# Performance work log

Hardware: AMD Instinct MI355X
Metric: run time of the kernel (lower is better)

## Reference

```python
import math
import jax, jax.numpy as jnp
import numpy as np

K = 4          # beats_per_bar
POS_DIM = 32   # fourier pos-embed dim


def setup_inputs() -> dict:
    key = jax.random.key(0)
    k1, k2, k3 = jax.random.split(key, 3)
    B, M, D = 8, 8192, 1024
    beat_emb = jax.random.normal(k1, (B, M, D), dtype=jnp.float32)
    W = jax.random.normal(k2, (D, D + POS_DIM), dtype=jnp.float32) * 0.02  # nn.Linear weight [out, in]
    b = jax.random.normal(k3, (D,), dtype=jnp.float32) * 0.02
    return {"beat_emb": beat_emb, "W": W, "b": b}


def _fourier_features(pos, dim):
    # pos: [Mb] in [0,1] -> [Mb, dim] (dim even, so no zero-pad branch needed)
    half = dim // 2
    freqs = jnp.exp(jnp.linspace(0.0, math.log(1000.0), half)).astype(pos.dtype)
    ang = pos[:, None] * freqs  # [Mb, half]
    return jnp.concatenate([jnp.sin(ang), jnp.cos(ang)], axis=-1)


def reference(beat_emb, W, b):
    B, M, D = beat_emb.shape
    Mb = (M + K - 1) // K
    pad = Mb * K - M
    x = jnp.pad(beat_emb, ((0, 0), (0, pad), (0, 0))) if pad else beat_emb
    # fused segment mean: [B, Mb, K, D] -> sum -> divide by actual segment length
    sums = x.reshape(B, Mb, K, D).sum(axis=2)
    counts = jnp.minimum(K, M - jnp.arange(Mb) * K).astype(beat_emb.dtype)  # [Mb]
    out = sums / counts[None, :, None]  # [B, Mb, D]
    # fourier positional features on normalized bar index (same for every batch row)
    idx = jnp.arange(Mb, dtype=beat_emb.dtype)
    pos = jnp.clip(idx / max(1, Mb - 1), 0.0, 1.0)
    ff = _fourier_features(pos, POS_DIM)                     # [Mb, POS_DIM]
    ff = jnp.broadcast_to(ff[None], (B, Mb, POS_DIM))
    h = jnp.concatenate([out, ff], axis=-1)                  # [B, Mb, D+POS_DIM]
    return jnp.einsum('bmi,oi->bmo', h, W) + b               # Linear: x @ W.T + b
```

## Files before the change

### kernel.cpp

```cpp
#include <hip/hip_runtime.h>
#include <math.h>
#include <stdint.h>
#include <stddef.h>

typedef short bf16x8 __attribute__((ext_vector_type(8)));
typedef short bf16x4 __attribute__((ext_vector_type(4)));
typedef float f32x4  __attribute__((ext_vector_type(4)));

#define BATCH   8
#define D       1024
#define POSD    32
#define WIN     1056
#define MBARS   2048
#define MROWS   16384
#define NOUT    1024

__device__ __forceinline__ short f2bf(float f) {
    unsigned u = __builtin_bit_cast(unsigned, f);
    u += 0x7fffu + ((u >> 16) & 1u);
    return (short)(u >> 16);
}

__device__ __forceinline__ void async_load16(const short* g, short* l) {
    __builtin_amdgcn_global_load_lds((__attribute__((address_space(1))) void*)g,
                                     (__attribute__((address_space(3))) void*)l,
                                     16, 0, 0);
}

__global__ __launch_bounds__(256) void prep2(const float* __restrict__ W,
                                             const float* __restrict__ bias,
                                             short* __restrict__ Wb,
                                             float* __restrict__ FFW) {
    const int t   = threadIdx.x;
    const int bid = blockIdx.x;
    if (bid < NOUT) {
        const float* wr = W + (size_t)bid * WIN;
        float4 v = ((const float4*)wr)[t];
        bf16x4 o = { f2bf(v.x), f2bf(v.y), f2bf(v.z), f2bf(v.w) };
        *(bf16x4*)(Wb + (size_t)bid * D + t * 4) = o;
    } else {
        const int mb0 = (bid - NOUT) * 8;
        __shared__ float ff[8][32];
        if (t < 32) {
            float fr = expf((float)(t & 15) * (6.907755278982137f / 15.0f));
#pragma unroll
            for (int e = 0; e < 8; ++e) {
                float pos = (float)(mb0 + e) * (1.0f / (float)(MBARS - 1));
                float ang = pos * fr;
                ff[e][t] = (t < 16) ? sinf(ang) : cosf(ang);
            }
        }
        __syncthreads();
#pragma unroll
        for (int u = 0; u < 4; ++u) {
            const int n = t + u * 256;
            const float* wp = W + (size_t)n * WIN + D;
            float4 wv[8];
#pragma unroll
            for (int blk = 0; blk < 8; ++blk) wv[blk] = ((const float4*)wp)[blk];
            const float bn = bias[n];
#pragma unroll
            for (int e = 0; e < 8; ++e) {
                float s = bn;
#pragma unroll
                for (int blk = 0; blk < 8; ++blk) {
                    s += ff[e][blk * 4 + 0] * wv[blk].x + ff[e][blk * 4 + 1] * wv[blk].y
                       + ff[e][blk * 4 + 2] * wv[blk].z + ff[e][blk * 4 + 3] * wv[blk].w;
                }
                FFW[(size_t)(mb0 + e) * NOUT + n] = s;
            }
        }
    }
}

__global__ __launch_bounds__(512, 2) void fused(const float* __restrict__ x,
                                                const short* __restrict__ Wb,
                                                const float* __restrict__ FFW,
                                                float* __restrict__ out) {
    __shared__ short As[64 * 64];
    __shared__ short Bs[1024 * 64];

    const int tid  = threadIdx.x;
    const int wave = tid >> 6;
    const int lane = tid & 63;
    const int m0   = blockIdx.x * 64;

    const int ra = tid >> 3;
    const int oa = tid & 7;
    const float* xg = x + (size_t)(m0 + ra) * 4096 + oa * 8;
    short* aw = As + ra * 64 + ((oa ^ (ra & 7)) << 3);
    const short* bg = Wb + (size_t)ra * D + ((oa ^ (ra & 7)) << 3);
    short* bl = Bs + wave * 512;

    const int r  = lane & 15;
    const int q  = lane >> 4;
    const int rx = r & 7;
    const short* afr = As + r * 64;
    const short* bfr = Bs + (wave * 128 + r) * 64;
    const int sl0 = ((q    ) ^ rx) << 3;
    const int sl1 = ((4 + q) ^ rx) << 3;

    f32x4 acc[4][8] = {};

    for (int k0 = 0; k0 < D; k0 += 64) {
        __syncthreads();
        float4 t00 = *(const float4*)(xg + k0);
        float4 t01 = *(const float4*)(xg + k0 + 4);
        float4 t10 = *(const float4*)(xg + k0 + 1024);
        float4 t11 = *(const float4*)(xg + k0 + 1028);
        float4 t20 = *(const float4*)(xg + k0 + 2048);
        float4 t21 = *(const float4*)(xg + k0 + 2052);
        float4 t30 = *(const float4*)(xg + k0 + 3072);
        float4 t31 = *(const float4*)(xg + k0 + 3076);
#pragma unroll
        for (int i = 0; i < 16; ++i)
            async_load16(bg + k0 + (size_t)i * 64 * D, bl + i * 4096);
        bf16x8 av = { f2bf((t00.x + t10.x + t20.x + t30.x) * 0.25f),
                      f2bf((t00.y + t10.y + t20.y + t30.y) * 0.25f),
                      f2bf((t00.z + t10.z + t20.z + t30.z) * 0.25f),
                      f2bf((t00.w + t10.w + t20.w + t30.w) * 0.25f),
                      f2bf((t01.x + t11.x + t21.x + t31.x) * 0.25f),
                      f2bf((t01.y + t11.y + t21.y + t31.y) * 0.25f),
                      f2bf((t01.z + t11.z + t21.z + t31.z) * 0.25f),
                      f2bf((t01.w + t11.w + t21.w + t31.w) * 0.25f) };
        *(bf16x8*)aw = av;
        __syncthreads();

#pragma unroll
        for (int s = 0; s < 2; ++s) {
            const int sl = s ? sl1 : sl0;
            bf16x8 a[4], b[8];
#pragma unroll
            for (int i = 0; i < 4; ++i) a[i] = *(const bf16x8*)(afr + i * 1024 + sl);
#pragma unroll
            for (int j = 0; j < 8; ++j) b[j] = *(const bf16x8*)(bfr + j * 1024 + sl);
#pragma unroll
            for (int i = 0; i < 4; ++i)
#pragma unroll
                for (int j = 0; j < 8; ++j)
                    acc[i][j] = __builtin_amdgcn_mfma_f32_16x16x32_bf16(a[i], b[j], acc[i][j], 0, 0, 0);
        }
    }

    const int mbb = m0 & (MBARS - 1);
    const int c0  = wave * 128 + r;
    const int rt0 = q << 2;
#pragma unroll
    for (int i = 0; i < 4; ++i)
#pragma unroll
        for (int rg = 0; rg < 4; ++rg) {
            const int rt = i * 16 + rt0 + rg;
            const float* fw = FFW + (size_t)(mbb + rt) * NOUT + c0;
            float* cp = out + (size_t)(m0 + rt) * NOUT + c0;
#pragma unroll
            for (int j = 0; j < 8; ++j)
                cp[j * 16] = acc[i][j][rg] + fw[j * 16];
        }
}

extern "C" void kernel_launch(void* const* d_in, const int* in_sizes, int n_in,
                              void* d_out, int out_size, void* d_ws, size_t ws_size,
                              hipStream_t stream) {
    const float* x    = (const float*)d_in[0];
    const float* W    = (const float*)d_in[1];
    const float* bias = (const float*)d_in[2];
    float* out = (float*)d_out;

    short* Wb  = (short*)d_ws;
    float* FFW = (float*)((char*)d_ws + (size_t)NOUT * D * sizeof(short));

    prep2<<<dim3(NOUT + MBARS / 8), dim3(256), 0, stream>>>(W, bias, Wb, FFW);
    fused<<<dim3(MROWS / 64), dim3(512), 0, stream>>>(x, Wb, FFW, out);
}
```

Measured before the change: 466.3 us.

## Double-buffer A tile and read W fragments directly from global memory

Drops the large LDS staging buffer for the bf16 weight matrix. Each wave now loads its B fragments straight from global memory (through L2 and cache). The pooled activation tile is double-buffered in LDS, so the next K-slice of x is fetched while the MFMAs run on the current one, and the loop needs only one barrier per iteration. This cuts LDS use a lot, which may allow higher occupancy. The cost is that every wave reissues uncoalesced-ish global loads for W on each iteration, with latency exposed to the MFMA loop.

```diff
diff --git a/kernel.cpp b/kernel.cpp
--- a/kernel.cpp
+++ b/kernel.cpp
@@ -19,12 +19,6 @@
     unsigned u = __builtin_bit_cast(unsigned, f);
     u += 0x7fffu + ((u >> 16) & 1u);
     return (short)(u >> 16);
-}
-
-__device__ __forceinline__ void async_load16(const short* g, short* l) {
-    __builtin_amdgcn_global_load_lds((__attribute__((address_space(1))) void*)g,
-                                     (__attribute__((address_space(3))) void*)l,
-                                     16, 0, 0);
 }
 
 __global__ __launch_bounds__(256) void prep2(const float* __restrict__ W,
@@ -77,8 +71,7 @@
                                                 const short* __restrict__ Wb,
                                                 const float* __restrict__ FFW,
                                                 float* __restrict__ out) {
-    __shared__ short As[64 * 64];
-    __shared__ short Bs[1024 * 64];
+    __shared__ short As[2][64 * 64];
 
     const int tid  = threadIdx.x;
     const int wave = tid >> 6;
@@ -88,58 +81,82 @@
     const int ra = tid >> 3;
     const int oa = tid & 7;
     const float* xg = x + (size_t)(m0 + ra) * 4096 + oa * 8;
-    short* aw = As + ra * 64 + ((oa ^ (ra & 7)) << 3);
-    const short* bg = Wb + (size_t)ra * D + ((oa ^ (ra & 7)) << 3);
-    short* bl = Bs + wave * 512;
+    const int aw = ra * 64 + ((oa ^ (ra & 7)) << 3);
 
     const int r  = lane & 15;
     const int q  = lane >> 4;
     const int rx = r & 7;
-    const short* afr = As + r * 64;
-    const short* bfr = Bs + (wave * 128 + r) * 64;
     const int sl0 = ((q    ) ^ rx) << 3;
     const int sl1 = ((4 + q) ^ rx) << 3;
 
+    const short* bj[8];
+#pragma unroll
+    for (int j = 0; j < 8; ++j)
+        bj[j] = Wb + (size_t)(wave * 128 + j * 16 + r) * 1024 + q * 8;
+
     f32x4 acc[4][8] = {};
 
-    for (int k0 = 0; k0 < D; k0 += 64) {
-        __syncthreads();
-        float4 t00 = *(const float4*)(xg + k0);
-        float4 t01 = *(const float4*)(xg + k0 + 4);
-        float4 t10 = *(const float4*)(xg + k0 + 1024);
-        float4 t11 = *(const float4*)(xg + k0 + 1028);
-        float4 t20 = *(const float4*)(xg + k0 + 2048);
-        float4 t21 = *(const float4*)(xg + k0 + 2052);
-        float4 t30 = *(const float4*)(xg + k0 + 3072);
-        float4 t31 = *(const float4*)(xg + k0 + 3076);
+    {
+        float4 X[8];
 #pragma unroll
-        for (int i = 0; i < 16; ++i)
-            async_load16(bg + k0 + (size_t)i * 64 * D, bl + i * 4096);
-        bf16x8 av = { f2bf((t00.x + t10.x + t20.x + t30.x) * 0.25f),
-                      f2bf((t00.y + t10.y + t20.y + t30.y) * 0.25f),
-                      f2bf((t00.z + t10.z + t20.z + t30.z) * 0.25f),
-                      f2bf((t00.w + t10.w + t20.w + t30.w) * 0.25f),
-                      f2bf((t01.x + t11.x + t21.x + t31.x) * 0.25f),
-                      f2bf((t01.y + t11.y + t21.y + t31.y) * 0.25f),
-                      f2bf((t01.z + t11.z + t21.z + t31.z) * 0.25f),
-                      f2bf((t01.w + t11.w + t21.w + t31.w) * 0.25f) };
-        *(bf16x8*)aw = av;
-        __syncthreads();
+        for (int bt = 0; bt < 4; ++bt) {
+            X[2 * bt]     = *(const float4*)(xg + bt * 1024);
+            X[2 * bt + 1] = *(const float4*)(xg + bt * 1024 + 4);
+        }
+        bf16x8 av = { f2bf((X[0].x + X[2].x + X[4].x + X[6].x) * 0.25f),
+                      f2bf((X[0].y + X[2].y + X[4].y + X[6].y) * 0.25f),
+                      f2bf((X[0].z + X[2].z + X[4].z + X[6].z) * 0.25f),
+                      f2bf((X[0].w + X[2].w + X[4].w + X[6].w) * 0.25f),
+                      f2bf((X[1].x + X[3].x + X[5].x + X[7].x) * 0.25f),
+                      f2bf((X[1].y + X[3].y + X[5].y + X[7].y) * 0.25f),
+                      f2bf((X[1].z + X[3].z + X[5].z + X[7].z) * 0.25f),
+                      f2bf((X[1].w + X[3].w + X[5].w + X[7].w) * 0.25f) };
+        *(bf16x8*)(&As[0][aw]) = av;
+    }
+    __syncthreads();
+
+#pragma unroll 2
+    for (int k = 0; k < 16; ++k) {
+        const short* ap = &As[k & 1][r * 64];
+        const int kof = k * 64;
+
+        float4 X[8];
+        if (k < 15) {
+            const float* xk = xg + (k + 1) * 64;
+#pragma unroll
+            for (int bt = 0; bt < 4; ++bt) {
+                X[2 * bt]     = *(const float4*)(xk + bt * 1024);
+                X[2 * bt + 1] = *(const float4*)(xk + bt * 1024 + 4);
+            }
+        }
 
 #pragma unroll
         for (int s = 0; s < 2; ++s) {
             const int sl = s ? sl1 : sl0;
             bf16x8 a[4], b[8];
 #pragma unroll
-            for (int i = 0; i < 4; ++i) a[i] = *(const bf16x8*)(afr + i * 1024 + sl);
+            for (int i = 0; i < 4; ++i) a[i] = *(const bf16x8*)(ap + i * 1024 + sl);
 #pragma unroll
-            for (int j = 0; j < 8; ++j) b[j] = *(const bf16x8*)(bfr + j * 1024 + sl);
+            for (int j = 0; j < 8; ++j) b[j] = *(const bf16x8*)(bj[j] + kof + s * 32);
 #pragma unroll
             for (int i = 0; i < 4; ++i)
 #pragma unroll
                 for (int j = 0; j < 8; ++j)
                     acc[i][j] = __builtin_amdgcn_mfma_f32_16x16x32_bf16(a[i], b[j], acc[i][j], 0, 0, 0);
         }
+
+        if (k < 15) {
+            bf16x8 av = { f2bf((X[0].x + X[2].x + X[4].x + X[6].x) * 0.25f),
+                          f2bf((X[0].y + X[2].y + X[4].y + X[6].y) * 0.25f),
+                          f2bf((X[0].z + X[2].z + X[4].z + X[6].z) * 0.25f),
+                          f2bf((X[0].w + X[2].w + X[4].w + X[6].w) * 0.25f),
+                          f2bf((X[1].x + X[3].x + X[5].x + X[7].x) * 0.25f),
+                          f2bf((X[1].y + X[3].y + X[5].y + X[7].y) * 0.25f),
+                          f2bf((X[1].z + X[3].z + X[5].z + X[7].z) * 0.25f),
+                          f2bf((X[1].w + X[3].w + X[5].w + X[7].w) * 0.25f) };
+            *(bf16x8*)(&As[(k + 1) & 1][aw]) = av;
+        }
+        __syncthreads();
     }
 
     const int mbb = m0 & (MBARS - 1);
```

Measured after the change: 514.1 us. 10.2% more time.
